# Kernel tuning notes

Hardware: AMD Instinct MI355X
Metric: run time of the kernel (lower is better)

The kernel has to match this reference:

```python
import jax, jax.numpy as jnp
import numpy as np

B, C, H, W = 256, 1024, 14, 14
C8 = C // 8
TXT = 150 * 1024  # flattened text embed dim
N = H * W  # 196, matches self.l shape (1,196)


def setup_inputs() -> dict:
    key = jax.random.key(0)
    ks = jax.random.split(key, 12)
    s = lambda fan_in: 1.0 / np.sqrt(fan_in)
    return {
        "x": jax.random.normal(ks[0], (B, C, H, W), jnp.float32),
        "text_embed": jax.random.normal(ks[1], (B, 1, 150, 1024), jnp.float32),
        "G_w": jax.random.normal(ks[2], (C, TXT), jnp.float32) * s(TXT),
        "G_b": jnp.zeros((C,), jnp.float32),
        "l": jax.random.normal(ks[3], (1, N), jnp.float32) * 0.02,
        "W_q": jax.random.normal(ks[4], (C8, C), jnp.float32) * s(C),
        "b_q": jnp.zeros((C8,), jnp.float32),
        "W_k": jax.random.normal(ks[5], (C8, C), jnp.float32) * s(C),
        "b_k": jnp.zeros((C8,), jnp.float32),
        "W_v": jax.random.normal(ks[6], (C, C), jnp.float32) * s(C),
        "b_v": jnp.zeros((C,), jnp.float32),
        "gamma": jnp.ones((1,), jnp.float32) * 0.5,
    }


def reference(x, text_embed, G_w, G_b, l, W_q, b_q, W_k, b_k, W_v, b_v, gamma):
    b, c, h, w = x.shape
    n = h * w
    # text preprocessing: squeeze(1) + flatten + Linear G -> (B, C)
    te = text_embed.reshape(b, -1) @ G_w.T + G_b  # (B, C)
    # bmm(te[:, :, None], l broadcast) == outer product per batch -> (B, C, N)
    te_flat = te[:, :, None] * l[None, 0, None, :]  # (B, C, N)
    x_flat = x.reshape(b, c, n)  # (B, C, N)
    # 1x1 convs == channel matmuls
    proj_query = jnp.einsum('qc,bcn->bnq', W_q, x_flat) + b_q  # (B, N, C8)
    proj_key = jnp.einsum('kc,bcn->bkn', W_k, te_flat) + b_k[None, :, None]  # (B, C8, N)
    energy = jnp.einsum('bnq,bqm->bnm', proj_query, proj_key)  # (B, N, N)
    attention = jax.nn.softmax(energy, axis=-1)  # (B, N, N)
    proj_value = jnp.einsum('vc,bcn->bvn', W_v, te_flat) + b_v[None, :, None]  # (B, C, N)
    # out = bmm(value, attention^T): out[b,c,m] = sum_n value[b,c,n] * attn[b,m,n]
    out = jnp.einsum('bcn,bmn->bcm', proj_value, attention)  # (B, C, N)
    out = out.reshape(b, c, h, w)
    return gamma * out + x
```

## Files before the change

### kernel.cpp

```cpp
#include <hip/hip_runtime.h>
#include <hip/hip_bf16.h>

#define BB 256
#define CC 1024
#define CQ 128
#define NN 196
#define TXTK 153600
#define SPLITS 64
#define KCHUNK 2400
#define KSTEPS 75
#define LDP 40

typedef __attribute__((ext_vector_type(8))) short short8;
typedef __attribute__((ext_vector_type(4))) float f32x4;

static __device__ __forceinline__ unsigned int pkbf(float a, float b) {
  __hip_bfloat162 t = __float22bfloat162_rn(make_float2(a, b));
  unsigned int r;
  __builtin_memcpy(&r, &t, 4);
  return r;
}

__global__ __launch_bounds__(1024) void k1_gemm_partial(
    const float* __restrict__ TE, const float* __restrict__ Gw,
    float* __restrict__ part) {
  __shared__ unsigned short Al[2][256 * LDP];
  __shared__ unsigned short Bl[2][256 * LDP];

  const int tid = threadIdx.x;
  const int fid = blockIdx.x;
  const int r8 = fid & 7;
  const int nt = (fid >> 3) & 3;
  const int sp = (fid >> 5) * 8 + r8;
  const int kbase = sp * KCHUNK;

  const int lane = tid & 63;
  const int w = tid >> 6;
  const int wm = w & 3;
  const int wn = w >> 2;

  const int r0 = tid >> 3;
  const int c0 = (tid & 7) * 4;
  const float* Ap0 = TE + (size_t)r0 * TXTK + kbase + c0;
  const float* Ap1 = TE + (size_t)(r0 + 128) * TXTK + kbase + c0;
  const float* Bp0 = Gw + (size_t)(nt * 256 + r0) * TXTK + kbase + c0;
  const float* Bp1 = Gw + (size_t)(nt * 256 + r0 + 128) * TXTK + kbase + c0;
  const int l0 = r0 * LDP + c0;
  const int l1 = (r0 + 128) * LDP + c0;

  f32x4 ra0, ra1, rb0, rb1;
  auto loadRegs = [&](int ko) {
    ra0 = *(const f32x4*)(Ap0 + ko);
    ra1 = *(const f32x4*)(Ap1 + ko);
    rb0 = *(const f32x4*)(Bp0 + ko);
    rb1 = *(const f32x4*)(Bp1 + ko);
  };
  auto cvt4 = [](f32x4 v) {
    uint2 h;
    h.x = pkbf(v.x, v.y);
    h.y = pkbf(v.z, v.w);
    return h;
  };
  auto writeLDS = [&](int buf) {
    *(uint2*)&Al[buf][l0] = cvt4(ra0);
    *(uint2*)&Al[buf][l1] = cvt4(ra1);
    *(uint2*)&Bl[buf][l0] = cvt4(rb0);
    *(uint2*)&Bl[buf][l1] = cvt4(rb1);
  };

  f32x4 acc[4][4];
  const f32x4 z = {0.f, 0.f, 0.f, 0.f};
#pragma unroll
  for (int i = 0; i < 4; ++i)
#pragma unroll
    for (int j = 0; j < 4; ++j) acc[i][j] = z;

  loadRegs(0);
  writeLDS(0);
  __syncthreads();

  const int k8 = (lane >> 4) * 8;
  const int fr = lane & 15;

  for (int ks = 0; ks < KSTEPS; ++ks) {
    const int cur = ks & 1;
    if (ks + 1 < KSTEPS) loadRegs((ks + 1) * 32);

    short8 bfr[4];
#pragma unroll
    for (int ns = 0; ns < 4; ++ns) {
      int col = wn * 64 + ns * 16 + fr;
      bfr[ns] = *(const short8*)&Bl[cur][col * LDP + k8];
    }
#pragma unroll
    for (int ms = 0; ms < 4; ++ms) {
      int row = wm * 64 + ms * 16 + fr;
      short8 af = *(const short8*)&Al[cur][row * LDP + k8];
#pragma unroll
      for (int ns = 0; ns < 4; ++ns)
        acc[ms][ns] = __builtin_amdgcn_mfma_f32_16x16x32_bf16(af, bfr[ns], acc[ms][ns], 0, 0, 0);
    }

    if (ks + 1 < KSTEPS) writeLDS(cur ^ 1);
    __syncthreads();
  }

  float* dst = part + (size_t)sp * (BB * CC);
#pragma unroll
  for (int ms = 0; ms < 4; ++ms)
#pragma unroll
    for (int ns = 0; ns < 4; ++ns)
#pragma unroll
      for (int j = 0; j < 4; ++j) {
        int b = wm * 64 + ms * 16 + (lane >> 4) * 4 + j;
        int c = nt * 256 + wn * 64 + ns * 16 + fr;
        dst[b * CC + c] = acc[ms][ns][j];
      }
}

__global__ __launch_bounds__(256) void k2_reduce(
    const float* __restrict__ part, const float* __restrict__ Gb,
    float* __restrict__ te) {
  const int gid = blockIdx.x * 256 + threadIdx.x;
  const f32x4* p = (const f32x4*)part;
  f32x4 s = *(const f32x4*)(Gb + ((gid * 4) & (CC - 1)));
#pragma unroll 4
  for (int sp = 0; sp < SPLITS; ++sp) s += p[(size_t)sp * (BB * CC / 4) + gid];
  ((f32x4*)te)[gid] = s;
}

__global__ __launch_bounds__(256) void k3_dual(
    const float* __restrict__ te, const float* __restrict__ Wk,
    const float* __restrict__ Wv, float* __restrict__ kbuf,
    float* __restrict__ vbuf) {
  __shared__ float As[64][33];
  __shared__ float Bs[64][33];
  const int tid = threadIdx.x;
  const int tx = tid & 15, ty = tid >> 4;
  const int bx = blockIdx.x;
  const float* Wt;
  float* outp;
  int Nout, n0;
  if (bx < 2) { Wt = Wk; outp = kbuf; Nout = CQ; n0 = bx * 64; }
  else        { Wt = Wv; outp = vbuf; Nout = CC; n0 = (bx - 2) * 64; }
  const int m0 = blockIdx.y * 64;
  float acc[4][4] = {};
  for (int k0 = 0; k0 < CC; k0 += 32) {
#pragma unroll
    for (int j = 0; j < 2; ++j) {
      int i = tid + 256 * j;
      int r = i >> 3, c4 = (i & 7) * 4;
      f32x4 va = *(const f32x4*)(te + (size_t)(m0 + r) * CC + k0 + c4);
      As[r][c4 + 0] = va.x; As[r][c4 + 1] = va.y; As[r][c4 + 2] = va.z; As[r][c4 + 3] = va.w;
      f32x4 vb4 = *(const f32x4*)(Wt + (size_t)(n0 + r) * CC + k0 + c4);
      Bs[r][c4 + 0] = vb4.x; Bs[r][c4 + 1] = vb4.y; Bs[r][c4 + 2] = vb4.z; Bs[r][c4 + 3] = vb4.w;
    }
    __syncthreads();
#pragma unroll 8
    for (int k = 0; k < 32; ++k) {
      float a[4], bv[4];
#pragma unroll
      for (int i = 0; i < 4; ++i) a[i] = As[ty * 4 + i][k];
#pragma unroll
      for (int j = 0; j < 4; ++j) bv[j] = Bs[tx * 4 + j][k];
#pragma unroll
      for (int i = 0; i < 4; ++i)
#pragma unroll
        for (int j = 0; j < 4; ++j) acc[i][j] += a[i] * bv[j];
    }
    __syncthreads();
  }
#pragma unroll
  for (int i = 0; i < 4; ++i)
#pragma unroll
    for (int j = 0; j < 4; ++j)
      outp[(size_t)(m0 + ty * 4 + i) * Nout + n0 + tx * 4 + j] = acc[i][j];
}

__global__ __launch_bounds__(1024) void k4a_attn(
    const float* __restrict__ x, const float* __restrict__ kb,
    const float* __restrict__ Wq, const float* __restrict__ bq,
    float* __restrict__ pbuf) {
  __shared__ float kbs[CQ];
  __shared__ float wqs[512];
  __shared__ float partl[16][NN];
  __shared__ float dsh;

  const int h = blockIdx.x;
  const int b = blockIdx.y;
  const int ch0 = h * 512;
  const int tid = threadIdx.x;

  if (tid < CQ) kbs[tid] = kb[b * CQ + tid];
  __syncthreads();

  if (tid < 512) {
    float s = 0.f;
#pragma unroll 8
    for (int q = 0; q < CQ; ++q) s += Wq[q * CC + ch0 + tid] * kbs[q];
    wqs[tid] = s;
  }
  if (tid == 1023) {
    float d = 0.f;
    if (h == 0)
      for (int q = 0; q < CQ; ++q) d += bq[q] * kbs[q];
    dsh = d;
  }
  __syncthreads();

  const float* xb = x + (size_t)b * (CC * NN) + (size_t)ch0 * NN;
  if (tid < 784) {
    const int r = tid / 49, n4 = tid % 49;
    f32x4 acc = {0.f, 0.f, 0.f, 0.f};
#pragma unroll 4
    for (int c = r; c < 512; c += 16) {
      f32x4 v = *(const f32x4*)(xb + c * NN + n4 * 4);
      acc += wqs[c] * v;
    }
    partl[r][n4 * 4 + 0] = acc.x;
    partl[r][n4 * 4 + 1] = acc.y;
    partl[r][n4 * 4 + 2] = acc.z;
    partl[r][n4 * 4 + 3] = acc.w;
  }
  __syncthreads();
  if (tid < NN) {
    float s = dsh;
#pragma unroll
    for (int r = 0; r < 16; ++r) s += partl[r][tid];
    pbuf[b * 400 + h * 200 + tid] = s;
  }
}

__global__ __launch_bounds__(256) void k4mid(
    const float* __restrict__ pbuf, const float* __restrict__ l,
    float* __restrict__ sbuf) {
  __shared__ float ls[NN];
  __shared__ float av[NN];
  const int b = blockIdx.x;
  const int tid = threadIdx.x;
  if (tid < NN) {
    ls[tid] = l[tid];
    av[tid] = pbuf[b * 400 + tid] + pbuf[b * 400 + 200 + tid];
  }
  __syncthreads();
  if (tid < NN) {
    const float a = av[tid];
    float m = -1e30f;
    for (int j = 0; j < NN; ++j) m = fmaxf(m, a * ls[j]);
    float num = 0.f, den = 0.f;
    for (int j = 0; j < NN; ++j) {
      float e = __expf(a * ls[j] - m);
      num += ls[j] * e;
      den += e;
    }
    sbuf[b * NN + tid] = num / den;
  }
}

__global__ __launch_bounds__(256) void k4b_epilogue(
    const float* __restrict__ x, const float* __restrict__ vbuf,
    const float* __restrict__ bv, const float* __restrict__ sbuf,
    const float* __restrict__ gammap, float* __restrict__ out) {
  __shared__ __align__(16) float sv[NN];
  __shared__ float Ac[128];
  __shared__ float Bc[128];
  const int sl = blockIdx.x;
  const int b = blockIdx.y;
  const int tid = threadIdx.x;
  const float g = gammap[0];

  if (tid < NN) sv[tid] = sbuf[b * NN + tid];
  if (tid < 128) {
    Ac[tid] = g * vbuf[b * CC + sl * 128 + tid];
    Bc[tid] = g * bv[sl * 128 + tid];
  }
  __syncthreads();

  const float* xb = x + (size_t)b * (CC * NN) + (size_t)sl * 128 * NN;
  float* ob = out + (size_t)b * (CC * NN) + (size_t)sl * 128 * NN;
  for (int f = tid; f < 6272; f += 256) {
    const int c = f / 49;
    const int n4 = f - c * 49;
    f32x4 xv = *(const f32x4*)(xb + f * 4);
    f32x4 s4 = *(const f32x4*)&sv[n4 * 4];
    f32x4 o = Ac[c] * s4 + (Bc[c] + xv);
    *(f32x4*)(ob + f * 4) = o;
  }
}

extern "C" void kernel_launch(void* const* d_in, const int* in_sizes, int n_in,
                              void* d_out, int out_size, void* d_ws, size_t ws_size,
                              hipStream_t stream) {
  const float* x    = (const float*)d_in[0];
  const float* TE   = (const float*)d_in[1];
  const float* Gw   = (const float*)d_in[2];
  const float* Gb   = (const float*)d_in[3];
  const float* l    = (const float*)d_in[4];
  const float* Wq   = (const float*)d_in[5];
  const float* bq   = (const float*)d_in[6];
  const float* Wk   = (const float*)d_in[7];
  const float* Wv   = (const float*)d_in[9];
  const float* bv   = (const float*)d_in[10];
  const float* gam  = (const float*)d_in[11];

  float* out  = (float*)d_out;
  float* part = out;
  float* pbuf = out + 20000000;
  float* te   = (float*)d_ws;
  float* kbuf = te + BB * CC;
  float* vbuf = kbuf + BB * CQ;
  float* sbuf = vbuf + BB * CC;

  hipLaunchKernelGGL(k1_gemm_partial, dim3(256), dim3(1024), 0, stream, TE, Gw, part);
  hipLaunchKernelGGL(k2_reduce, dim3(256), dim3(256), 0, stream, part, Gb, te);
  hipLaunchKernelGGL(k3_dual, dim3(18, 4), dim3(256), 0, stream, te, Wk, Wv, kbuf, vbuf);
  hipLaunchKernelGGL(k4a_attn, dim3(2, BB), dim3(1024), 0, stream, x, kbuf, Wq, bq, pbuf);
  hipLaunchKernelGGL(k4mid, dim3(BB), dim3(256), 0, stream, pbuf, l, sbuf);
  hipLaunchKernelGGL(k4b_epilogue, dim3(8, BB), dim3(256), 0, stream, x, vbuf, bv, sbuf, gam, out);
}
```

Before: 424.0 us.

## Retile split-K text GEMM to 256x128 tiles with 512-thread blocks

The split-K GEMM kernel changes from 256 blocks of 1024 threads, each computing a 256x256 output tile, to 512 blocks of 512 threads, each computing a 256x128 tile. The grid index mapping is reordered so the N-tile is the slowest-varying index, and the LDS row padding shrinks from 40 to 36 elements. The goal is more resident blocks per CU and better scheduling of the 64 K-splits. In exchange, each block reuses the TE tile over fewer outputs, so total global reads of TE double, and the new padding may change LDS bank conflicts.

```diff
diff --git a/kernel.cpp b/kernel.cpp
--- a/kernel.cpp
+++ b/kernel.cpp
@@ -9,7 +9,7 @@
 #define SPLITS 64
 #define KCHUNK 2400
 #define KSTEPS 75
-#define LDP 40
+#define LDP 36
 
 typedef __attribute__((ext_vector_type(8))) short short8;
 typedef __attribute__((ext_vector_type(4))) float f32x4;
@@ -21,17 +21,18 @@
   return r;
 }
 
-__global__ __launch_bounds__(1024) void k1_gemm_partial(
+__global__ __launch_bounds__(512) void k1_gemm_partial(
     const float* __restrict__ TE, const float* __restrict__ Gw,
     float* __restrict__ part) {
   __shared__ unsigned short Al[2][256 * LDP];
-  __shared__ unsigned short Bl[2][256 * LDP];
+  __shared__ unsigned short Bl[2][128 * LDP];
 
   const int tid = threadIdx.x;
   const int fid = blockIdx.x;
-  const int r8 = fid & 7;
-  const int nt = (fid >> 3) & 3;
-  const int sp = (fid >> 5) * 8 + r8;
+  const int spl = fid & 7;
+  const int sph = (fid >> 3) & 7;
+  const int nt = fid >> 6;
+  const int sp = sph * 8 + spl;
   const int kbase = sp * KCHUNK;
 
   const int lane = tid & 63;
@@ -41,19 +42,20 @@
 
   const int r0 = tid >> 3;
   const int c0 = (tid & 7) * 4;
-  const float* Ap0 = TE + (size_t)r0 * TXTK + kbase + c0;
-  const float* Ap1 = TE + (size_t)(r0 + 128) * TXTK + kbase + c0;
-  const float* Bp0 = Gw + (size_t)(nt * 256 + r0) * TXTK + kbase + c0;
-  const float* Bp1 = Gw + (size_t)(nt * 256 + r0 + 128) * TXTK + kbase + c0;
-  const int l0 = r0 * LDP + c0;
-  const int l1 = (r0 + 128) * LDP + c0;
-
-  f32x4 ra0, ra1, rb0, rb1;
+  int arow[4], brow[2];
+#pragma unroll
+  for (int j = 0; j < 4; ++j) arow[j] = r0 + 64 * j;
+#pragma unroll
+  for (int j = 0; j < 2; ++j) brow[j] = r0 + 64 * j;
+
+  f32x4 ra[4], rb[2];
   auto loadRegs = [&](int ko) {
-    ra0 = *(const f32x4*)(Ap0 + ko);
-    ra1 = *(const f32x4*)(Ap1 + ko);
-    rb0 = *(const f32x4*)(Bp0 + ko);
-    rb1 = *(const f32x4*)(Bp1 + ko);
+#pragma unroll
+    for (int j = 0; j < 4; ++j)
+      ra[j] = *(const f32x4*)(TE + (size_t)arow[j] * TXTK + kbase + ko + c0);
+#pragma unroll
+    for (int j = 0; j < 2; ++j)
+      rb[j] = *(const f32x4*)(Gw + (size_t)(nt * 128 + brow[j]) * TXTK + kbase + ko + c0);
   };
   auto cvt4 = [](f32x4 v) {
     uint2 h;
@@ -62,10 +64,12 @@
     return h;
   };
   auto writeLDS = [&](int buf) {
-    *(uint2*)&Al[buf][l0] = cvt4(ra0);
-    *(uint2*)&Al[buf][l1] = cvt4(ra1);
-    *(uint2*)&Bl[buf][l0] = cvt4(rb0);
-    *(uint2*)&Bl[buf][l1] = cvt4(rb1);
+#pragma unroll
+    for (int j = 0; j < 4; ++j)
+      *(uint2*)&Al[buf][arow[j] * LDP + c0] = cvt4(ra[j]);
+#pragma unroll
+    for (int j = 0; j < 2; ++j)
+      *(uint2*)&Bl[buf][brow[j] * LDP + c0] = cvt4(rb[j]);
   };
 
   f32x4 acc[4][4];
@@ -113,7 +117,7 @@
 #pragma unroll
       for (int j = 0; j < 4; ++j) {
         int b = wm * 64 + ms * 16 + (lane >> 4) * 4 + j;
-        int c = nt * 256 + wn * 64 + ns * 16 + fr;
+        int c = nt * 128 + wn * 64 + ns * 16 + fr;
         dst[b * CC + c] = acc[ms][ns][j];
       }
 }
@@ -311,7 +315,7 @@
   float* vbuf = kbuf + BB * CQ;
   float* sbuf = vbuf + BB * CC;
 
-  hipLaunchKernelGGL(k1_gemm_partial, dim3(256), dim3(1024), 0, stream, TE, Gw, part);
+  hipLaunchKernelGGL(k1_gemm_partial, dim3(512), dim3(512), 0, stream, TE, Gw, part);
   hipLaunchKernelGGL(k2_reduce, dim3(256), dim3(256), 0, stream, part, Gb, te);
   hipLaunchKernelGGL(k3_dual, dim3(18, 4), dim3(256), 0, stream, te, Wk, Wv, kbuf, vbuf);
   hipLaunchKernelGGL(k4a_attn, dim3(2, BB), dim3(1024), 0, stream, x, kbuf, Wq, bq, pbuf);
```

After: 434.8 us. 1.03x slower.

## Store split-K partials as bf16 in fragment layout and add nontemporal accesses

Applied to the files above, without the earlier changes.

The split-K GEMM now packs its partial sums to bf16 and writes them in the MFMA fragment order as contiguous 8-byte vectors, which halves partial-buffer traffic and makes the stores coalesced. The reduce kernel is rewritten to read that layout, accumulate in fp32, and scatter the results back to te with the bias added. Nontemporal loads for G_w and nontemporal stores for the epilogue output are also added to limit cache pollution. Rounding the partials to bf16 adds some numeric error to te.

```diff
diff --git a/kernel.cpp b/kernel.cpp
--- a/kernel.cpp
+++ b/kernel.cpp
@@ -13,6 +13,7 @@
 
 typedef __attribute__((ext_vector_type(8))) short short8;
 typedef __attribute__((ext_vector_type(4))) float f32x4;
+typedef __attribute__((ext_vector_type(2))) unsigned int u32x2;
 
 static __device__ __forceinline__ unsigned int pkbf(float a, float b) {
   __hip_bfloat162 t = __float22bfloat162_rn(make_float2(a, b));
@@ -21,9 +22,22 @@
   return r;
 }
 
+static __device__ __forceinline__ float bflo(unsigned int u) {
+  unsigned int v = u << 16;
+  float f;
+  __builtin_memcpy(&f, &v, 4);
+  return f;
+}
+static __device__ __forceinline__ float bfhi(unsigned int u) {
+  unsigned int v = u & 0xffff0000u;
+  float f;
+  __builtin_memcpy(&f, &v, 4);
+  return f;
+}
+
 __global__ __launch_bounds__(1024) void k1_gemm_partial(
     const float* __restrict__ TE, const float* __restrict__ Gw,
-    float* __restrict__ part) {
+    unsigned int* __restrict__ part) {
   __shared__ unsigned short Al[2][256 * LDP];
   __shared__ unsigned short Bl[2][256 * LDP];
 
@@ -52,8 +66,8 @@
   auto loadRegs = [&](int ko) {
     ra0 = *(const f32x4*)(Ap0 + ko);
     ra1 = *(const f32x4*)(Ap1 + ko);
-    rb0 = *(const f32x4*)(Bp0 + ko);
-    rb1 = *(const f32x4*)(Bp1 + ko);
+    rb0 = __builtin_nontemporal_load((const f32x4*)(Bp0 + ko));
+    rb1 = __builtin_nontemporal_load((const f32x4*)(Bp1 + ko));
   };
   auto cvt4 = [](f32x4 v) {
     uint2 h;
@@ -105,28 +119,46 @@
     __syncthreads();
   }
 
-  float* dst = part + (size_t)sp * (BB * CC);
+  u32x2* d2 = (u32x2*)part + (size_t)(sp * 4 + nt) * 16384;
 #pragma unroll
   for (int ms = 0; ms < 4; ++ms)
 #pragma unroll
-    for (int ns = 0; ns < 4; ++ns)
-#pragma unroll
-      for (int j = 0; j < 4; ++j) {
-        int b = wm * 64 + ms * 16 + (lane >> 4) * 4 + j;
-        int c = nt * 256 + wn * 64 + ns * 16 + fr;
-        dst[b * CC + c] = acc[ms][ns][j];
-      }
-}
-
-__global__ __launch_bounds__(256) void k2_reduce(
-    const float* __restrict__ part, const float* __restrict__ Gb,
+    for (int ns = 0; ns < 4; ++ns) {
+      u32x2 pk;
+      pk.x = pkbf(acc[ms][ns][0], acc[ms][ns][1]);
+      pk.y = pkbf(acc[ms][ns][2], acc[ms][ns][3]);
+      const int v = ms * 4 + ns;
+      __builtin_nontemporal_store(pk, d2 + v * 1024 + tid);
+    }
+}
+
+__global__ __launch_bounds__(1024) void k2_reduce(
+    const unsigned int* __restrict__ part, const float* __restrict__ Gb,
     float* __restrict__ te) {
-  const int gid = blockIdx.x * 256 + threadIdx.x;
-  const f32x4* p = (const f32x4*)part;
-  f32x4 s = *(const f32x4*)(Gb + ((gid * 4) & (CC - 1)));
+  const int idx = blockIdx.x * 1024 + threadIdx.x;
+  const int nt = idx >> 14;
+  const int s = idx & 16383;
+  const u32x2* p2 = (const u32x2*)part;
+
+  float a0 = 0.f, a1 = 0.f, a2 = 0.f, a3 = 0.f;
 #pragma unroll 4
-  for (int sp = 0; sp < SPLITS; ++sp) s += p[(size_t)sp * (BB * CC / 4) + gid];
-  ((f32x4*)te)[gid] = s;
+  for (int sp = 0; sp < SPLITS; ++sp) {
+    u32x2 u = p2[(size_t)(sp * 4 + nt) * 16384 + s];
+    a0 += bflo(u.x); a1 += bfhi(u.x);
+    a2 += bflo(u.y); a3 += bfhi(u.y);
+  }
+
+  const int v = s >> 10, t = s & 1023;
+  const int lane = t & 63, w = t >> 6;
+  const int wm = w & 3, wn = w >> 2;
+  const int ms = v >> 2, ns = v & 3;
+  const int b0 = wm * 64 + ms * 16 + (lane >> 4) * 4;
+  const int c = nt * 256 + wn * 64 + ns * 16 + (lane & 15);
+  const float gb = Gb[c];
+  te[(size_t)(b0 + 0) * CC + c] = a0 + gb;
+  te[(size_t)(b0 + 1) * CC + c] = a1 + gb;
+  te[(size_t)(b0 + 2) * CC + c] = a2 + gb;
+  te[(size_t)(b0 + 3) * CC + c] = a3 + gb;
 }
 
 __global__ __launch_bounds__(256) void k3_dual(
@@ -284,7 +316,7 @@
     f32x4 xv = *(const f32x4*)(xb + f * 4);
     f32x4 s4 = *(const f32x4*)&sv[n4 * 4];
     f32x4 o = Ac[c] * s4 + (Bc[c] + xv);
-    *(f32x4*)(ob + f * 4) = o;
+    __builtin_nontemporal_store(o, (f32x4*)(ob + f * 4));
   }
 }
 
@@ -304,7 +336,7 @@
   const float* gam  = (const float*)d_in[11];
 
   float* out  = (float*)d_out;
-  float* part = out;
+  unsigned int* part = (unsigned int*)d_out;
   float* pbuf = out + 20000000;
   float* te   = (float*)d_ws;
   float* kbuf = te + BB * CC;
@@ -312,7 +344,7 @@
   float* sbuf = vbuf + BB * CC;
 
   hipLaunchKernelGGL(k1_gemm_partial, dim3(256), dim3(1024), 0, stream, TE, Gw, part);
-  hipLaunchKernelGGL(k2_reduce, dim3(256), dim3(256), 0, stream, part, Gb, te);
+  hipLaunchKernelGGL(k2_reduce, dim3(64), dim3(1024), 0, stream, part, Gb, te);
   hipLaunchKernelGGL(k3_dual, dim3(18, 4), dim3(256), 0, stream, te, Wk, Wv, kbuf, vbuf);
   hipLaunchKernelGGL(k4a_attn, dim3(2, BB), dim3(1024), 0, stream, x, kbuf, Wq, bq, pbuf);
   hipLaunchKernelGGL(k4mid, dim3(BB), dim3(256), 0, stream, pbuf, l, sbuf);
```

New measurement: 388.7 us. 8.3% less time.
